# Kernel tuning notes

Hardware: AMD Instinct MI355X
Metric: run time of the kernel (lower is better)

The kernel has to match this reference:

```python
import jax, jax.numpy as jnp
import numpy as np

D = 2048
H = 16
HD = D // H  # 128
B, L, LP = 2, 2048, 2048


def setup_inputs() -> dict:
    key = jax.random.key(0)
    ks = jax.random.split(key, 9)
    s = 1.0 / np.sqrt(D)
    return {
        "x": jax.random.normal(ks[0], (B, L, D), jnp.float32),
        "past_k": jax.random.normal(ks[1], (B, H, LP, HD), jnp.float32),
        "past_v": jax.random.normal(ks[2], (B, H, LP, HD), jnp.float32),
        "Wq": jax.random.normal(ks[3], (D, D), jnp.float32) * s,
        "bq": jnp.zeros((D,), jnp.float32),
        "Wk": jax.random.normal(ks[4], (D, D), jnp.float32) * s,
        "bk": jnp.zeros((D,), jnp.float32),
        "Wv": jax.random.normal(ks[5], (D, D), jnp.float32) * s,
        "bv": jnp.zeros((D,), jnp.float32),
        "Wo": jax.random.normal(ks[6], (D, D), jnp.float32) * s,
        "bo": jnp.zeros((D,), jnp.float32),
    }


def _split_heads(t):
    b, l, d = t.shape
    return t.reshape(b, l, H, HD).transpose(0, 2, 1, 3)  # [B,H,L,Hd]


def reference(x, past_k, past_v, Wq, bq, Wk, bk, Wv, bv, Wo, bo):
    # torch Linear: y = x @ W.T + b
    q = _split_heads(x @ Wq.T + bq)                 # [B,H,L,Hd]
    k_new = _split_heads(x @ Wk.T + bk)
    v_new = _split_heads(x @ Wv.T + bv)
    k = jnp.concatenate([past_k, k_new], axis=2)    # [B,H,Lp+L,Hd]
    v = jnp.concatenate([past_v, v_new], axis=2)
    scale = 1.0 / jnp.sqrt(jnp.asarray(HD, x.dtype))
    scores = jnp.einsum('bhqd,bhkd->bhqk', q, k) * scale  # [B,H,L,Lp+L]
    attn = jax.nn.softmax(scores, axis=-1)
    ctx = jnp.einsum('bhqk,bhkd->bhqd', attn, v)    # [B,H,L,Hd]
    merged = ctx.transpose(0, 2, 1, 3).reshape(x.shape[0], x.shape[1], D)
    out = merged @ Wo.T + bo
    return (out, k, v)
```

## Files before the change

kernel.cpp:

```cpp
#include <hip/hip_runtime.h>
#include <cstdint>
#include <cstddef>

typedef __bf16 bf16;
typedef __bf16 bf16x8 __attribute__((ext_vector_type(8)));
typedef __bf16 bf16x4 __attribute__((ext_vector_type(4)));
typedef float f32x4 __attribute__((ext_vector_type(4)));
typedef unsigned int uint;

#define D_MODEL 2048
#define NH 16
#define HD 128
#define LQ 2048
#define LT 4096

__device__ __forceinline__ void gload16(const void* g, void* l) {
  __builtin_amdgcn_global_load_lds((const __attribute__((address_space(1))) void*)g,
                                   (__attribute__((address_space(3))) void*)l, 16, 0, 0);
}

__global__ __launch_bounds__(256) void prep(const float* __restrict__ x,
                                            const float* __restrict__ Wq, const float* __restrict__ Wk,
                                            const float* __restrict__ Wv, const float* __restrict__ Wo,
                                            const float* __restrict__ pk, const float* __restrict__ pv,
                                            bf16* __restrict__ xb, bf16* __restrict__ wb,
                                            float* __restrict__ kout, bf16* __restrict__ kbf,
                                            float* __restrict__ vout) {
  const int bid = blockIdx.x;
  if (bid < 8192) {
    int i = (bid * 256 + threadIdx.x) * 4;
    float4 v = *(const float4*)(x + i);
    bf16x4 o = { (bf16)v.x, (bf16)v.y, (bf16)v.z, (bf16)v.w };
    *(bf16x4*)(xb + i) = o;
  } else if (bid < 24576) {
    const int r = bid - 8192;
    const int z = r >> 12;
    const float* s = (z == 0) ? Wq : (z == 1) ? Wk : (z == 2) ? Wv : Wo;
    int i = ((r & 4095) * 256 + threadIdx.x) * 4;
    float4 v = *(const float4*)(s + i);
    bf16x4 o = { (bf16)v.x, (bf16)v.y, (bf16)v.z, (bf16)v.w };
    *(bf16x4*)(wb + (size_t)z * 4194304 + i) = o;
  } else if (bid < 32768) {
    int i = ((bid - 24576) * 256 + threadIdx.x) * 4;
    int bh = i >> 18;
    int rem = i & 262143;
    size_t o = ((size_t)bh << 19) + rem;
    float4 v = *(const float4*)(pk + i);
    *(float4*)(kout + o) = v;
    bf16x4 ob = { (bf16)v.x, (bf16)v.y, (bf16)v.z, (bf16)v.w };
    *(bf16x4*)(kbf + o) = ob;
  } else {
    int i = ((bid - 32768) * 256 + threadIdx.x) * 4;
    int bh = i >> 18;
    int rem = i & 262143;
    size_t o = ((size_t)bh << 19) + rem;
    float4 v = *(const float4*)(pv + i);
    *(float4*)(vout + o) = v;
  }
}

__global__ __launch_bounds__(256, 2) void qkv_gemm128(const bf16* __restrict__ xb, const bf16* __restrict__ wb,
    const float* __restrict__ bq, const float* __restrict__ bk, const float* __restrict__ bv,
    bf16* __restrict__ qb, float* __restrict__ kout, float* __restrict__ vout, bf16* __restrict__ kbf) {
  __shared__ alignas(16) bf16 sA[2][128 * 64];
  __shared__ alignas(16) bf16 sB[2][128 * 64];
  const int tid = threadIdx.x, lane = tid & 63, w = tid >> 6;
  const int fr = lane & 15, fg = lane >> 4;
  const int wm = (w >> 1) * 64, wn = (w & 1) * 64;
  const int flat = blockIdx.x;
  const int swz = (flat & 7) * 192 + (flat >> 3);
  const int z = swz >> 9;
  const int idx = swz & 511;
  const int n0 = (idx & 15) * 128;
  const int m0 = (idx >> 4) * 128;
  const bf16* A = xb;
  const bf16* Bw = wb + (size_t)z * 4194304;
  f32x4 acc[4][4];
#pragma unroll
  for (int a = 0; a < 4; a++)
#pragma unroll
    for (int b = 0; b < 4; b++) acc[a][b] = (f32x4){0.f, 0.f, 0.f, 0.f};

#define STG(k0s, buf) do {                                                                   \
    _Pragma("unroll")                                                                        \
    for (int j = 0; j < 4; j++) {                                                            \
      const int c_ = j * 256 + tid;                                                          \
      const int rS = c_ >> 3;                                                                \
      const int gS = (c_ & 7) ^ (rS & 7);                                                    \
      gload16(A  + (size_t)(m0 + rS) * 2048 + (k0s) + gS * 8,                                \
              &sA[buf][(j * 256 + (tid & 192)) * 8]);                                        \
      gload16(Bw + (size_t)(n0 + rS) * 2048 + (k0s) + gS * 8,                                \
              &sB[buf][(j * 256 + (tid & 192)) * 8]);                                        \
    }                                                                                        \
  } while (0)

  STG(0, 0);
  STG(64, 1);
  for (int t = 0; t < 32; ++t) {
    const int bsel = t & 1;
    asm volatile("s_waitcnt vmcnt(8)\n\ts_barrier" ::: "memory");
    bf16x8 af[2][4], bfr[2][4];
#pragma unroll
    for (int kk = 0; kk < 2; kk++) {
#pragma unroll
      for (int ni = 0; ni < 4; ni++) {
        const int row = wn + ni * 16 + fr;
        bfr[kk][ni] = *(const bf16x8*)(&sB[bsel][row * 64 + (((kk * 4 + fg) ^ (row & 7)) * 8)]);
      }
#pragma unroll
      for (int mi = 0; mi < 4; mi++) {
        const int row = wm + mi * 16 + fr;
        af[kk][mi] = *(const bf16x8*)(&sA[bsel][row * 64 + (((kk * 4 + fg) ^ (row & 7)) * 8)]);
      }
    }
    asm volatile("s_waitcnt lgkmcnt(0)\n\ts_barrier" ::: "memory");
    const int ks = ((t + 2) * 64) & 2047;
    STG(ks, bsel);
    __builtin_amdgcn_s_setprio(1);
#pragma unroll
    for (int kk = 0; kk < 2; kk++)
#pragma unroll
      for (int mi = 0; mi < 4; mi++)
#pragma unroll
        for (int ni = 0; ni < 4; ni++)
          acc[mi][ni] = __builtin_amdgcn_mfma_f32_16x16x32_bf16(af[kk][mi], bfr[kk][ni], acc[mi][ni], 0, 0, 0);
    __builtin_amdgcn_s_setprio(0);
  }
#undef STG
  asm volatile("s_waitcnt vmcnt(0)" ::: "memory");
  const float* bias = (z == 0) ? bq : (z == 1 ? bk : bv);
#pragma unroll
  for (int ni = 0; ni < 4; ni++) {
    const int col = n0 + wn + ni * 16 + fr;
    const float bi = bias[col];
#pragma unroll
    for (int mi = 0; mi < 4; mi++) {
#pragma unroll
      for (int r = 0; r < 4; r++) {
        const int row = m0 + wm + mi * 16 + fg * 4 + r;
        float v = acc[mi][ni][r] + bi;
        if (z == 0) {
          qb[(size_t)row * 2048 + col] = (bf16)(v * 0.12751744955867606f);
        } else {
          size_t co = (((size_t)(row >> 11) * 16 + (col >> 7)) * 4096 + 2048 + (row & 2047)) * 128 + (col & 127);
          if (z == 1) { kout[co] = v; kbf[co] = (bf16)v; }
          else        { vout[co] = v; }
        }
      }
    }
  }
}

__global__ __launch_bounds__(256) void build_vt(const float* __restrict__ vsrc, bf16* __restrict__ vtb) {
  __shared__ float tile[64][65];
  const int tid = threadIdx.x;
  const int bh = blockIdx.z;
  const int t0 = blockIdx.x * 64, d0 = blockIdx.y * 64;
  const float* src = vsrc + ((size_t)bh * LT + t0) * HD + d0;
#pragma unroll
  for (int i = 0; i < 4; i++) {
    int idx = i * 256 + tid;
    int rr = idx >> 4, c4 = (idx & 15) * 4;
    float4 v = *(const float4*)(src + rr * HD + c4);
    tile[rr][c4 + 0] = v.x; tile[rr][c4 + 1] = v.y; tile[rr][c4 + 2] = v.z; tile[rr][c4 + 3] = v.w;
  }
  __syncthreads();
  bf16* dst = vtb + (size_t)bh * HD * LT + (size_t)d0 * LT + t0;
#pragma unroll
  for (int i = 0; i < 4; i++) {
    int idx = i * 256 + tid;
    int dr = idx >> 4, c4 = (idx & 15) * 4;
    bf16x4 o = { (bf16)tile[c4 + 0][dr], (bf16)tile[c4 + 1][dr],
                 (bf16)tile[c4 + 2][dr], (bf16)tile[c4 + 3][dr] };
    *(bf16x4*)(dst + (size_t)dr * LT + c4) = o;
  }
}

__global__ __launch_bounds__(256, 1) void attn(const bf16* __restrict__ qb, const bf16* __restrict__ kb,
                                               const bf16* __restrict__ vtb, bf16* __restrict__ ctxb) {
  __shared__ alignas(16) bf16 kbuf[2][64 * 128];
  __shared__ alignas(16) bf16 vtbuf[2][128 * 64];
  const int tid = threadIdx.x, lane = tid & 63, w = tid >> 6;
  const int fr = lane & 15, fg = lane >> 4;
  const int i_ = blockIdx.x + 8 * blockIdx.y;
  const int j_ = i_ >> 3;
  const int bh = (i_ & 7) * 4 + (j_ & 3);
  const int q0 = (j_ >> 2) * 256;
  const int b = bh >> 4;
  bf16x8 aq[4][4];
#pragma unroll
  for (int s = 0; s < 4; s++) {
    const bf16* qrow = qb + (size_t)(b * LQ + q0 + w * 64 + s * 16 + fr) * D_MODEL + (bh & 15) * HD;
#pragma unroll
    for (int c = 0; c < 4; c++) aq[s][c] = *(const bf16x8*)(qrow + c * 32 + fg * 8);
  }
  const bf16* Kb = kb + (size_t)bh * LT * HD;
  const bf16* Vt = vtb + (size_t)bh * HD * LT;
  f32x4 ctx[4][8], sum_[4];
#pragma unroll
  for (int s = 0; s < 4; s++) {
#pragma unroll
    for (int d = 0; d < 8; d++) ctx[s][d] = (f32x4){0.f, 0.f, 0.f, 0.f};
    sum_[s] = (f32x4){0.f, 0.f, 0.f, 0.f};
  }
  bf16x8 vones;
#pragma unroll
  for (int j = 0; j < 8; j++) vones[j] = (bf16)1.0f;

#define STAGE_KV(k0s, sel)                                                                   \
  do {                                                                                       \
    _Pragma("unroll")                                                                        \
    for (int j = 0; j < 4; j++) {                                                            \
      const int krow = j * 16 + w * 4 + (lane >> 4);                                         \
      const int kscol = ((lane & 15) ^ (krow & 7)) * 8;                                      \
      gload16(Kb + (size_t)((k0s) + krow) * HD + kscol, &kbuf[sel][(j * 16 + w * 4) * HD]);  \
      const int vrw = j * 32 + w * 8 + (lane >> 3);                                          \
      const int vscol = ((lane & 7) ^ (vrw & 7)) * 8;                                        \
      gload16(Vt + (size_t)vrw * LT + (k0s) + vscol, &vtbuf[sel][(j * 32 + w * 8) * 64]);    \
    }                                                                                        \
  } while (0)

  STAGE_KV(0, 0);
  int sel = 0;
  for (int k0 = 0; k0 < LT; k0 += 64) {
    __syncthreads();
    const int kn = (k0 + 64) & (LT - 1);
    STAGE_KV(kn, sel ^ 1);
    const bf16* kcur = &kbuf[sel][0];
    const bf16* vcur = &vtbuf[sel][0];
    f32x4 sS[4][4];
    __builtin_amdgcn_s_setprio(1);
#pragma unroll
    for (int n = 0; n < 4; n++) {
#pragma unroll
      for (int s = 0; s < 4; s++) sS[s][n] = (f32x4){0.f, 0.f, 0.f, 0.f};
#pragma unroll
      for (int c = 0; c < 4; c++) {
        bf16x8 kf = *(const bf16x8*)(kcur + (n * 16 + fr) * HD + (((c * 4 + fg) ^ (fr & 7)) * 8));
#pragma unroll
        for (int s = 0; s < 4; s++)
          sS[s][n] = __builtin_amdgcn_mfma_f32_16x16x32_bf16(kf, aq[s][c], sS[s][n], 0, 0, 0);
      }
    }
    __builtin_amdgcn_s_setprio(0);
    bf16x8 pf[4][2];
#pragma unroll
    for (int s = 0; s < 4; s++) {
      uint Dd[4][2];
#pragma unroll
      for (int n = 0; n < 4; n++) {
        uint hb[4];
#pragma unroll
        for (int r = 0; r < 4; r++) {
          bf16 h = (bf16)__builtin_amdgcn_exp2f(sS[s][n][r]);
          unsigned short us;
          __builtin_memcpy(&us, &h, 2);
          hb[r] = us;
        }
        Dd[n][0] = hb[0] | (hb[1] << 16);
        Dd[n][1] = hb[2] | (hb[3] << 16);
      }
#pragma unroll
      for (int c = 0; c < 2; c++) {
        uint T[4];
#pragma unroll
        for (int p = 0; p < 2; p++) {
          uint a = Dd[2 * c][p], b2 = Dd[2 * c + 1][p];
          asm("v_permlane32_swap_b32 %0, %1" : "+v"(a), "+v"(b2));
          asm("v_permlane16_swap_b32 %0, %1" : "+v"(a), "+v"(b2));
          T[p] = a; T[2 + p] = b2;
        }
        union { uint u[4]; bf16x8 v; } cv;
        cv.u[0] = T[0]; cv.u[1] = T[1]; cv.u[2] = T[2]; cv.u[3] = T[3];
        pf[s][c] = cv.v;
      }
    }
    __builtin_amdgcn_s_setprio(1);
#pragma unroll
    for (int d = 0; d < 8; d++) {
      bf16x8 v0 = *(const bf16x8*)(vcur + (d * 16 + fr) * 64 + ((fg ^ (fr & 7)) * 8));
#pragma unroll
      for (int s = 0; s < 4; s++)
        ctx[s][d] = __builtin_amdgcn_mfma_f32_16x16x32_bf16(pf[s][0], v0, ctx[s][d], 0, 0, 0);
      bf16x8 v1 = *(const bf16x8*)(vcur + (d * 16 + fr) * 64 + (((4 + fg) ^ (fr & 7)) * 8));
#pragma unroll
      for (int s = 0; s < 4; s++)
        ctx[s][d] = __builtin_amdgcn_mfma_f32_16x16x32_bf16(pf[s][1], v1, ctx[s][d], 0, 0, 0);
    }
#pragma unroll
    for (int s = 0; s < 4; s++) {
      sum_[s] = __builtin_amdgcn_mfma_f32_16x16x32_bf16(pf[s][0], vones, sum_[s], 0, 0, 0);
      sum_[s] = __builtin_amdgcn_mfma_f32_16x16x32_bf16(pf[s][1], vones, sum_[s], 0, 0, 0);
    }
    __builtin_amdgcn_s_setprio(0);
    sel ^= 1;
  }
#undef STAGE_KV
#pragma unroll
  for (int s = 0; s < 4; s++) {
    float inv[4];
#pragma unroll
    for (int r = 0; r < 4; r++) inv[r] = 1.f / sum_[s][r];
    bf16* crow = ctxb + (size_t)(b * LQ + q0 + w * 64 + s * 16 + fg * 4) * D_MODEL + (bh & 15) * HD + fr;
#pragma unroll
    for (int r = 0; r < 4; r++)
#pragma unroll
      for (int d = 0; d < 8; d++)
        crow[(size_t)r * D_MODEL + d * 16] = (bf16)(ctx[s][d][r] * inv[r]);
  }
}

__global__ __launch_bounds__(256, 2) void out_gemm(const bf16* __restrict__ cb, const bf16* __restrict__ wo,
                                                   const float* __restrict__ bo, float* __restrict__ out) {
  __shared__ alignas(16) bf16 sA[2][128 * 64];
  __shared__ alignas(16) bf16 sB[2][128 * 64];
  const int tid = threadIdx.x, lane = tid & 63, w = tid >> 6;
  const int fr = lane & 15, fg = lane >> 4;
  const int wm = (w >> 1) * 64, wn = (w & 1) * 64;
  const int flat = blockIdx.x;
  const int swz = (flat & 7) * 64 + (flat >> 3);
  const int n0 = (swz & 15) * 128;
  const int m0 = (swz >> 4) * 128;
  const bf16* A = cb;
  const bf16* Bw = wo;
  f32x4 acc[4][4];
#pragma unroll
  for (int a = 0; a < 4; a++)
#pragma unroll
    for (int b = 0; b < 4; b++) acc[a][b] = (f32x4){0.f, 0.f, 0.f, 0.f};

#define STG(k0s, buf) do {                                                                   \
    _Pragma("unroll")                                                                        \
    for (int j = 0; j < 4; j++) {                                                            \
      const int c_ = j * 256 + tid;                                                          \
      const int rS = c_ >> 3;                                                                \
      const int gS = (c_ & 7) ^ (rS & 7);                                                    \
      gload16(A  + (size_t)(m0 + rS) * 2048 + (k0s) + gS * 8,                                \
              &sA[buf][(j * 256 + (tid & 192)) * 8]);                                        \
      gload16(Bw + (size_t)(n0 + rS) * 2048 + (k0s) + gS * 8,                                \
              &sB[buf][(j * 256 + (tid & 192)) * 8]);                                        \
    }                                                                                        \
  } while (0)

  STG(0, 0);
  STG(64, 1);
  for (int t = 0; t < 32; ++t) {
    const int bsel = t & 1;
    asm volatile("s_waitcnt vmcnt(8)\n\ts_barrier" ::: "memory");
    bf16x8 af[2][4], bfr[2][4];
#pragma unroll
    for (int kk = 0; kk < 2; kk++) {
#pragma unroll
      for (int ni = 0; ni < 4; ni++) {
        const int row = wn + ni * 16 + fr;
        bfr[kk][ni] = *(const bf16x8*)(&sB[bsel][row * 64 + (((kk * 4 + fg) ^ (row & 7)) * 8)]);
      }
#pragma unroll
      for (int mi = 0; mi < 4; mi++) {
        const int row = wm + mi * 16 + fr;
        af[kk][mi] = *(const bf16x8*)(&sA[bsel][row * 64 + (((kk * 4 + fg) ^ (row & 7)) * 8)]);
      }
    }
    asm volatile("s_waitcnt lgkmcnt(0)\n\ts_barrier" ::: "memory");
    const int ks = ((t + 2) * 64) & 2047;
    STG(ks, bsel);
    __builtin_amdgcn_s_setprio(1);
#pragma unroll
    for (int kk = 0; kk < 2; kk++)
#pragma unroll
      for (int mi = 0; mi < 4; mi++)
#pragma unroll
        for (int ni = 0; ni < 4; ni++)
          acc[mi][ni] = __builtin_amdgcn_mfma_f32_16x16x32_bf16(af[kk][mi], bfr[kk][ni], acc[mi][ni], 0, 0, 0);
    __builtin_amdgcn_s_setprio(0);
  }
#undef STG
  asm volatile("s_waitcnt vmcnt(0)" ::: "memory");
#pragma unroll
  for (int ni = 0; ni < 4; ni++) {
    int col = n0 + wn + ni * 16 + fr;
    float bi = bo[col];
#pragma unroll
    for (int mi = 0; mi < 4; mi++)
#pragma unroll
      for (int r = 0; r < 4; r++) {
        int row = m0 + wm + mi * 16 + fg * 4 + r;
        out[(size_t)row * 2048 + col] = acc[mi][ni][r] + bi;
      }
  }
}

extern "C" void kernel_launch(void* const* d_in, const int* in_sizes, int n_in,
                              void* d_out, int out_size, void* d_ws, size_t ws_size,
                              hipStream_t stream) {
  const float* x  = (const float*)d_in[0];
  const float* pk = (const float*)d_in[1];
  const float* pv = (const float*)d_in[2];
  const float* Wq = (const float*)d_in[3];
  const float* bq = (const float*)d_in[4];
  const float* Wk = (const float*)d_in[5];
  const float* bk = (const float*)d_in[6];
  const float* Wv = (const float*)d_in[7];
  const float* bv = (const float*)d_in[8];
  const float* Wo = (const float*)d_in[9];
  const float* bo = (const float*)d_in[10];

  float* out  = (float*)d_out;
  float* kout = out + 8388608;
  float* vout = out + 25165824;

  char* p = (char*)d_ws;
  bf16* xb  = (bf16*)p;
  bf16* wb  = (bf16*)(p + 16777216);
  bf16* qb  = (bf16*)(p + 50331648);
  bf16* kbf = (bf16*)(p + 67108864);
  bf16* vtb = (bf16*)(p + 100663296);
  bf16* ctxb = xb;

  prep<<<40960, 256, 0, stream>>>(x, Wq, Wk, Wv, Wo, pk, pv, xb, wb, kout, kbf, vout);
  qkv_gemm128<<<1536, 256, 0, stream>>>(xb, wb, bq, bk, bv, qb, kout, vout, kbf);
  build_vt<<<dim3(64, 2, 32), 256, 0, stream>>>(vout, vtb);
  attn<<<dim3(8, 32), 256, 0, stream>>>(qb, kbf, vtb, ctxb);
  out_gemm<<<512, 256, 0, stream>>>(ctxb, wb + 12582912, bo, out);
}
```

Measured before the change: 419.0 us.

## Split attention key tile across two wave groups with LDS reduction

The attention kernel now launches 512 threads per block. Two groups of four waves each handle half of every 64-key tile, and the partial context and row sums are combined through LDS at the end. V staging is deferred until after the QK^T MFMAs so the loads overlap compute. This doubles the waves available to hide latency on each CU, at the cost of an extra reduction step, more syncs and duplicated Q fragments per wave.

```diff
diff --git a/kernel.cpp b/kernel.cpp
--- a/kernel.cpp
+++ b/kernel.cpp
@@ -176,12 +176,14 @@
   }
 }
 
-__global__ __launch_bounds__(256, 1) void attn(const bf16* __restrict__ qb, const bf16* __restrict__ kb,
+__global__ __launch_bounds__(512, 2) void attn(const bf16* __restrict__ qb, const bf16* __restrict__ kb,
                                                const bf16* __restrict__ vtb, bf16* __restrict__ ctxb) {
   __shared__ alignas(16) bf16 kbuf[2][64 * 128];
   __shared__ alignas(16) bf16 vtbuf[2][128 * 64];
   const int tid = threadIdx.x, lane = tid & 63, w = tid >> 6;
   const int fr = lane & 15, fg = lane >> 4;
+  const int half = w >> 2;
+  const int g = w & 3;
   const int i_ = blockIdx.x + 8 * blockIdx.y;
   const int j_ = i_ >> 3;
   const int bh = (i_ & 7) * 4 + (j_ & 3);
@@ -190,7 +192,7 @@
   bf16x8 aq[4][4];
 #pragma unroll
   for (int s = 0; s < 4; s++) {
-    const bf16* qrow = qb + (size_t)(b * LQ + q0 + w * 64 + s * 16 + fr) * D_MODEL + (bh & 15) * HD;
+    const bf16* qrow = qb + (size_t)(b * LQ + q0 + g * 64 + s * 16 + fr) * D_MODEL + (bh & 15) * HD;
 #pragma unroll
     for (int c = 0; c < 4; c++) aq[s][c] = *(const bf16x8*)(qrow + c * 32 + fg * 8);
   }
@@ -207,106 +209,136 @@
 #pragma unroll
   for (int j = 0; j < 8; j++) vones[j] = (bf16)1.0f;
 
-#define STAGE_KV(k0s, sel)                                                                   \
+#define STAGE_K(k0s, sel)                                                                    \
   do {                                                                                       \
     _Pragma("unroll")                                                                        \
-    for (int j = 0; j < 4; j++) {                                                            \
-      const int krow = j * 16 + w * 4 + (lane >> 4);                                         \
+    for (int j = 0; j < 2; j++) {                                                            \
+      const int krow = j * 32 + w * 4 + (lane >> 4);                                         \
       const int kscol = ((lane & 15) ^ (krow & 7)) * 8;                                      \
-      gload16(Kb + (size_t)((k0s) + krow) * HD + kscol, &kbuf[sel][(j * 16 + w * 4) * HD]);  \
-      const int vrw = j * 32 + w * 8 + (lane >> 3);                                          \
-      const int vscol = ((lane & 7) ^ (vrw & 7)) * 8;                                        \
-      gload16(Vt + (size_t)vrw * LT + (k0s) + vscol, &vtbuf[sel][(j * 32 + w * 8) * 64]);    \
+      gload16(Kb + (size_t)((k0s) + krow) * HD + kscol, &kbuf[sel][(j * 32 + w * 4) * HD]);  \
     }                                                                                        \
   } while (0)
-
-  STAGE_KV(0, 0);
+#define STAGE_V(k0s, sel)                                                                    \
+  do {                                                                                       \
+    _Pragma("unroll")                                                                        \
+    for (int j = 0; j < 2; j++) {                                                            \
+      const int vrw = j * 64 + w * 8 + (lane >> 3);                                          \
+      const int vscol = ((lane & 7) ^ (vrw & 7)) * 8;                                        \
+      gload16(Vt + (size_t)vrw * LT + (k0s) + vscol, &vtbuf[sel][(j * 64 + w * 8) * 64]);    \
+    }                                                                                        \
+  } while (0)
+
+  STAGE_K(0, 0);
+  STAGE_V(0, 0);
   int sel = 0;
   for (int k0 = 0; k0 < LT; k0 += 64) {
     __syncthreads();
     const int kn = (k0 + 64) & (LT - 1);
-    STAGE_KV(kn, sel ^ 1);
+    STAGE_K(kn, sel ^ 1);
     const bf16* kcur = &kbuf[sel][0];
     const bf16* vcur = &vtbuf[sel][0];
-    f32x4 sS[4][4];
+    f32x4 sS[4][2];
     __builtin_amdgcn_s_setprio(1);
 #pragma unroll
-    for (int n = 0; n < 4; n++) {
-#pragma unroll
-      for (int s = 0; s < 4; s++) sS[s][n] = (f32x4){0.f, 0.f, 0.f, 0.f};
+    for (int nn = 0; nn < 2; nn++) {
+      const int n = half * 2 + nn;
+#pragma unroll
+      for (int s = 0; s < 4; s++) sS[s][nn] = (f32x4){0.f, 0.f, 0.f, 0.f};
 #pragma unroll
       for (int c = 0; c < 4; c++) {
         bf16x8 kf = *(const bf16x8*)(kcur + (n * 16 + fr) * HD + (((c * 4 + fg) ^ (fr & 7)) * 8));
 #pragma unroll
         for (int s = 0; s < 4; s++)
-          sS[s][n] = __builtin_amdgcn_mfma_f32_16x16x32_bf16(kf, aq[s][c], sS[s][n], 0, 0, 0);
+          sS[s][nn] = __builtin_amdgcn_mfma_f32_16x16x32_bf16(kf, aq[s][c], sS[s][nn], 0, 0, 0);
       }
     }
     __builtin_amdgcn_s_setprio(0);
-    bf16x8 pf[4][2];
+    STAGE_V(kn, sel ^ 1);
+    bf16x8 pf[4];
 #pragma unroll
     for (int s = 0; s < 4; s++) {
-      uint Dd[4][2];
-#pragma unroll
-      for (int n = 0; n < 4; n++) {
+      uint Dd[2][2];
+#pragma unroll
+      for (int nn = 0; nn < 2; nn++) {
         uint hb[4];
 #pragma unroll
         for (int r = 0; r < 4; r++) {
-          bf16 h = (bf16)__builtin_amdgcn_exp2f(sS[s][n][r]);
+          bf16 h = (bf16)__builtin_amdgcn_exp2f(sS[s][nn][r]);
           unsigned short us;
           __builtin_memcpy(&us, &h, 2);
           hb[r] = us;
         }
-        Dd[n][0] = hb[0] | (hb[1] << 16);
-        Dd[n][1] = hb[2] | (hb[3] << 16);
-      }
-#pragma unroll
-      for (int c = 0; c < 2; c++) {
-        uint T[4];
-#pragma unroll
-        for (int p = 0; p < 2; p++) {
-          uint a = Dd[2 * c][p], b2 = Dd[2 * c + 1][p];
-          asm("v_permlane32_swap_b32 %0, %1" : "+v"(a), "+v"(b2));
-          asm("v_permlane16_swap_b32 %0, %1" : "+v"(a), "+v"(b2));
-          T[p] = a; T[2 + p] = b2;
-        }
-        union { uint u[4]; bf16x8 v; } cv;
-        cv.u[0] = T[0]; cv.u[1] = T[1]; cv.u[2] = T[2]; cv.u[3] = T[3];
-        pf[s][c] = cv.v;
-      }
+        Dd[nn][0] = hb[0] | (hb[1] << 16);
+        Dd[nn][1] = hb[2] | (hb[3] << 16);
+      }
+      uint T[4];
+#pragma unroll
+      for (int p = 0; p < 2; p++) {
+        uint a = Dd[0][p], b2 = Dd[1][p];
+        asm("v_permlane32_swap_b32 %0, %1" : "+v"(a), "+v"(b2));
+        asm("v_permlane16_swap_b32 %0, %1" : "+v"(a), "+v"(b2));
+        T[p] = a; T[2 + p] = b2;
+      }
+      union { uint u[4]; bf16x8 v; } cv;
+      cv.u[0] = T[0]; cv.u[1] = T[1]; cv.u[2] = T[2]; cv.u[3] = T[3];
+      pf[s] = cv.v;
     }
     __builtin_amdgcn_s_setprio(1);
 #pragma unroll
     for (int d = 0; d < 8; d++) {
-      bf16x8 v0 = *(const bf16x8*)(vcur + (d * 16 + fr) * 64 + ((fg ^ (fr & 7)) * 8));
+      bf16x8 vf = *(const bf16x8*)(vcur + (d * 16 + fr) * 64 + (((half * 4 + fg) ^ (fr & 7)) * 8));
 #pragma unroll
       for (int s = 0; s < 4; s++)
-        ctx[s][d] = __builtin_amdgcn_mfma_f32_16x16x32_bf16(pf[s][0], v0, ctx[s][d], 0, 0, 0);
-      bf16x8 v1 = *(const bf16x8*)(vcur + (d * 16 + fr) * 64 + (((4 + fg) ^ (fr & 7)) * 8));
-#pragma unroll
-      for (int s = 0; s < 4; s++)
-        ctx[s][d] = __builtin_amdgcn_mfma_f32_16x16x32_bf16(pf[s][1], v1, ctx[s][d], 0, 0, 0);
-    }
-#pragma unroll
-    for (int s = 0; s < 4; s++) {
-      sum_[s] = __builtin_amdgcn_mfma_f32_16x16x32_bf16(pf[s][0], vones, sum_[s], 0, 0, 0);
-      sum_[s] = __builtin_amdgcn_mfma_f32_16x16x32_bf16(pf[s][1], vones, sum_[s], 0, 0, 0);
-    }
+        ctx[s][d] = __builtin_amdgcn_mfma_f32_16x16x32_bf16(pf[s], vf, ctx[s][d], 0, 0, 0);
+    }
+#pragma unroll
+    for (int s = 0; s < 4; s++)
+      sum_[s] = __builtin_amdgcn_mfma_f32_16x16x32_bf16(pf[s], vones, sum_[s], 0, 0, 0);
     __builtin_amdgcn_s_setprio(0);
     sel ^= 1;
   }
-#undef STAGE_KV
-#pragma unroll
-  for (int s = 0; s < 4; s++) {
-    float inv[4];
-#pragma unroll
-    for (int r = 0; r < 4; r++) inv[r] = 1.f / sum_[s][r];
-    bf16* crow = ctxb + (size_t)(b * LQ + q0 + w * 64 + s * 16 + fg * 4) * D_MODEL + (bh & 15) * HD + fr;
-#pragma unroll
-    for (int r = 0; r < 4; r++)
-#pragma unroll
-      for (int d = 0; d < 8; d++)
-        crow[(size_t)r * D_MODEL + d * 16] = (bf16)(ctx[s][d][r] * inv[r]);
+#undef STAGE_K
+#undef STAGE_V
+  asm volatile("s_waitcnt vmcnt(0)" ::: "memory");
+  __syncthreads();
+  {
+    float* redc = (float*)&kbuf[0][0];
+    float* reds = redc + 4 * 64 * 36;
+#pragma unroll
+    for (int s = 0; s < 4; s++) {
+      if (half == 1) {
+        float* dst = redc + (g * 64 + lane) * 36;
+#pragma unroll
+        for (int d = 0; d < 8; d++) *(f32x4*)(dst + d * 4) = ctx[s][d];
+        *(f32x4*)(reds + (g * 64 + lane) * 4) = sum_[s];
+      }
+      __syncthreads();
+      if (half == 0) {
+        const float* src = redc + (g * 64 + lane) * 36;
+#pragma unroll
+        for (int d = 0; d < 8; d++) {
+          f32x4 t = *(const f32x4*)(src + d * 4);
+          ctx[s][d] += t;
+        }
+        f32x4 ts = *(const f32x4*)(reds + (g * 64 + lane) * 4);
+        sum_[s] += ts;
+      }
+      __syncthreads();
+    }
+  }
+  if (half == 0) {
+#pragma unroll
+    for (int s = 0; s < 4; s++) {
+      float inv[4];
+#pragma unroll
+      for (int r = 0; r < 4; r++) inv[r] = 1.f / sum_[s][r];
+      bf16* crow = ctxb + (size_t)(b * LQ + q0 + g * 64 + s * 16 + fg * 4) * D_MODEL + (bh & 15) * HD + fr;
+#pragma unroll
+      for (int r = 0; r < 4; r++)
+#pragma unroll
+        for (int d = 0; d < 8; d++)
+          crow[(size_t)r * D_MODEL + d * 16] = (bf16)(ctx[s][d][r] * inv[r]);
+    }
   }
 }
 
@@ -420,6 +452,6 @@
   prep<<<40960, 256, 0, stream>>>(x, Wq, Wk, Wv, Wo, pk, pv, xb, wb, kout, kbf, vout);
   qkv_gemm128<<<1536, 256, 0, stream>>>(xb, wb, bq, bk, bv, qb, kout, vout, kbf);
   build_vt<<<dim3(64, 2, 32), 256, 0, stream>>>(vout, vtb);
-  attn<<<dim3(8, 32), 256, 0, stream>>>(qb, kbf, vtb, ctxb);
+  attn<<<dim3(8, 32), 512, 0, stream>>>(qb, kbf, vtb, ctxb);
   out_gemm<<<512, 256, 0, stream>>>(ctxb, wb + 12582912, bo, out);
 }
```

Measured after the change: 439.2 us. 4.8% more time.
